# Performance work log

Hardware: AMD Instinct MI355X
Metric: run time of the kernel (lower is better)

## Reference

```python
import jax, jax.numpy as jnp
import numpy as np

N_RBF = 32
EPS_DIST = 0.01
R_RBF_MAX = 5.0
POWERS = (1.0, -1.0)


def _rbf_features(dist):
    # dist: [..., ] -> [..., N_RBF]; Gaussian-on-distance 'soft one-hot'
    q = jnp.linspace(0.0, 1.0, N_RBF).astype(dist.dtype)
    mu = q ** 2 * R_RBF_MAX
    sigma = (1.0 + R_RBF_MAX * q) / 7.0
    d = dist[..., None]
    return d ** 2 * jnp.exp(-d - ((d - mu) / sigma) ** 2)


def _pair_features(diff, dist):
    # RBF (32) + distance powers (2) + raw differences (3) = 37 features
    f_dist = jnp.stack(
        [dist ** n if n > 0 else 1.0 / (dist ** (-n) + EPS_DIST) for n in POWERS],
        axis=-1,
    )
    return jnp.concatenate([_rbf_features(dist), f_dist, diff], axis=-1)


def _mlp(x, Ws, bs):
    # MLP with linear_out=False: activation applied after every layer incl. last
    for W, b in zip(Ws, bs):
        x = jax.nn.silu(x @ W + b)
    return x


def setup_inputs() -> dict:
    key = jax.random.key(0)
    ks = jax.random.split(key, 6)
    B, N, M = 2048, 32, 8
    D_PAIR = N_RBF + 2 + 3  # 37
    H, F1, F_ION = 128, 128, 32
    r = jax.random.normal(ks[0], (B, N, 3), jnp.float32) * 2.0
    R = jax.random.normal(ks[1], (M, 3), jnp.float32) * 3.0
    Z = jnp.arange(1, M + 1, dtype=jnp.float32)
    init = lambda k, s: (jax.random.normal(k, s, jnp.float32) / np.sqrt(s[0])).astype(jnp.float32)
    return dict(
        r=r, R=R, Z=Z,
        W0=init(ks[2], (D_PAIR, H)), b0=jnp.zeros((H,), jnp.float32),
        W1=init(ks[3], (H, F1)), b1=jnp.zeros((F1,), jnp.float32),
        Wion=init(ks[4], (1, F_ION)), bion=jnp.zeros((F_ION,), jnp.float32),
    )


def reference(r, R, Z, W0, b0, W1, b1, Wion, bion):
    B, N = r.shape[0], r.shape[1]
    # --- pairwise diffs / distances ---
    diff_el_el = r[..., :, None, :] - r[..., None, :, :]          # [B,N,N,3]
    eye = jnp.eye(N, dtype=r.dtype)
    # safe sqrt on the diagonal (grad-safe), diagonal distance forced to 0
    dist_el_el = jnp.sqrt(jnp.sum(diff_el_el ** 2, axis=-1) + eye) * (1.0 - eye)  # [B,N,N]
    diff_el_ion = r[..., :, None, :] - R                           # [B,N,M,3]
    dist_el_ion = jnp.sqrt(jnp.sum(diff_el_ion ** 2, axis=-1))     # [B,N,M]

    # --- per-edge features ---
    features_el_el = _pair_features(diff_el_el, dist_el_el)        # [B,N,N,37]
    features_el_ion = _pair_features(diff_el_ion, dist_el_ion)     # [B,N,M,37]

    # --- edge MLP + sum aggregation over ions ---
    h = _mlp(features_el_ion, [W0, W1], [b0, b1])                  # [B,N,M,128]
    one_el = jnp.sum(h, axis=-2)                                   # [B,N,128]
    concat_ei = jnp.reshape(features_el_ion, features_el_ion.shape[:-2] + (-1,))  # [B,N,M*37]
    features_el = jnp.concatenate([one_el, concat_ei], axis=-1)    # [B,N,128+M*37]

    # --- ion features ---
    Zt = jnp.tile(Z, (B, 1))                                       # [B,M]
    features_ion = jax.nn.silu(Zt[..., None] @ Wion + bion)        # [B,M,32]
    return (features_el, features_ion)
```

## Files before the change

### kernel.cpp

```cpp
#include <hip/hip_runtime.h>


typedef __attribute__((ext_vector_type(8))) short short8;
typedef __attribute__((ext_vector_type(4))) float f32x4;

#define ITERS     8
#define UNITS_IT  16
#define ROWLEN    424
#define OUT_EL    27787264

__device__ __forceinline__ unsigned short f2bf(float f){
    unsigned int u = __builtin_bit_cast(unsigned int, f);
    u += 0x7fffu + ((u >> 16) & 1u);
    return (unsigned short)(u >> 16);
}
__device__ __forceinline__ unsigned int cvtpk_bf16(float lo, float hi){
    unsigned int r;
    asm("v_cvt_pk_bf16_f32 %0, %1, %2" : "=v"(r) : "v"(lo), "v"(hi));
    return r;
}
__device__ __forceinline__ unsigned short bf16s(float x){
    return (unsigned short)cvtpk_bf16(x, x);
}
__device__ __forceinline__ float fast_silu(float x){
    return x * __builtin_amdgcn_rcpf(1.0f + __expf(-x));
}

__global__ __launch_bounds__(512, 4)
void el_kernel(const float* __restrict__ r,
               const float* __restrict__ Rion,
               const float* __restrict__ W0,
               const float* __restrict__ b0,
               const float* __restrict__ W1,
               const float* __restrict__ b1,
               float* __restrict__ out)
{
    __shared__ __align__(16) unsigned short W0L[8][2][64][8];
    __shared__ __align__(16) unsigned short W1L[8][4][64][8];
    __shared__ __align__(16) unsigned short UNI[8][2048];

    const int t    = threadIdx.x;
    const int lane = t & 63;
    const int w    = t >> 6;
    const int quad = lane >> 4;
    const int l16  = lane & 15;

    for (int i = t; i < 8*2*64*8; i += 512){
        int j = i & 7, ln = (i >> 3) & 63, ch = (i >> 9) & 1, tc = i >> 10;
        int q = ln >> 4, n = tc*16 + (ln & 15);
        float v = 0.f;
        if (ch == 0)            v = W0[(q*8 + j)*128 + n];
        else if (q == 0){
            if      (j < 5)     v = W0[(32 + j)*128 + n];
            else if (j == 5)    v = b0[n];
        }
        ((unsigned short*)W0L)[i] = f2bf(v);
    }
    for (int i = t; i < 8*4*64*8; i += 512){
        int j = i & 7, ln = (i >> 3) & 63, c = (i >> 9) & 3, tc = i >> 11;
        int k = c*32 + (ln >> 4)*8 + j, n = tc*16 + (ln & 15);
        ((unsigned short*)W1L)[i] = f2bf(W1[k*128 + n]);
    }
    if (t < 128){
        UNI[t >> 4][512 + (t & 15)*8 + 5] = 0x3F80;
        UNI[t >> 4][512 + (t & 15)*8 + 6] = 0;
        UNI[t >> 4][512 + (t & 15)*8 + 7] = 0;
    }

    const int frow  = t >> 2;
    const int phase = t & 3;
    const int ul    = frow >> 3;
    const int m     = frow & 7;
    const int e16   = frow & 15;
    const float Rx = Rion[m*3+0];
    const float Ry = Rion[m*3+1];
    const float Rz = Rion[m*3+2];

    unsigned short* const uw = &UNI[w][0];
    const int h0row = l16 * 128;
    const int swz   = (l16 & 7) << 3;

    const f32x4 zeroc = {0.f,0.f,0.f,0.f};

    float bias1[8];
    #pragma unroll
    for (int tc = 0; tc < 8; ++tc) bias1[tc] = b1[tc*16 + l16];

    __syncthreads();

    const int ubase0 = blockIdx.x * (UNITS_IT * ITERS);

    for (int it = 0; it < ITERS; ++it){
        const int ubase = ubase0 + it * UNITS_IT;

        {
            int gu = ubase + ul;
            float dx = r[gu*3+0] - Rx;
            float dy = r[gu*3+1] - Ry;
            float dz = r[gu*3+2] - Rz;
            float d2 = dx*dx + dy*dy + dz*dz;
            float d  = __builtin_amdgcn_sqrtf(d2);
            float* orow = &out[(size_t)gu*ROWLEN + 128 + m*37];
            for (int f = phase; f < 37; f += 4){
                float val;
                if (f < 32){
                    float q  = (float)f * (1.0f/31.0f);
                    float mu = q*q*5.0f;
                    float is = 7.0f * __builtin_amdgcn_rcpf(1.0f + 5.0f*q);
                    float uu = (d - mu) * is;
                    val = d2 * __expf(-d - uu*uu);
                } else if (f == 32) val = d;
                else if (f == 33)   val = __builtin_amdgcn_rcpf(d + 0.01f);
                else if (f == 34)   val = dx;
                else if (f == 35)   val = dy;
                else                val = dz;
                orow[f] = val;
                unsigned short ub = bf16s(val);
                if (f < 32) uw[(f >> 3)*128 + e16*8 + (f & 7)] = ub;
                else        uw[512 + e16*8 + (f - 32)]          = ub;
            }
            if (phase == 3) uw[512 + e16*8 + 5] = 0x3F80;
        }

        short8 bf0 = *(const short8*)&uw[quad*128 + l16*8];
        short8 bf1 = *(const short8*)&uw[512 + l16*8];
        #pragma unroll
        for (int tc = 0; tc < 8; ++tc){
            short8 a0 = *(const short8*)&W0L[tc][0][lane][0];
            short8 a1 = *(const short8*)&W0L[tc][1][lane][0];
            f32x4 acc = __builtin_amdgcn_mfma_f32_16x16x32_bf16(a0, bf0, zeroc, 0, 0, 0);
            acc       = __builtin_amdgcn_mfma_f32_16x16x32_bf16(a1, bf1, acc,   0, 0, 0);
            unsigned int p01 = cvtpk_bf16(fast_silu(acc[0]), fast_silu(acc[1]));
            unsigned int p23 = cvtpk_bf16(fast_silu(acc[2]), fast_silu(acc[3]));
            unsigned long long pk = (unsigned long long)p01 |
                                    ((unsigned long long)p23 << 32);
            *(unsigned long long*)&uw[h0row + ((tc*16 + quad*4) ^ swz)] = pk;
        }

        short8 afk[4];
        #pragma unroll
        for (int c = 0; c < 4; ++c)
            afk[c] = *(const short8*)&uw[h0row + ((c*32 + quad*8) ^ swz)];

        f32x4 acc1[8];
        #pragma unroll
        for (int i = 0; i < 8; ++i) acc1[i] = zeroc;
        #pragma unroll
        for (int c = 0; c < 4; ++c){
            #pragma unroll
            for (int tc = 0; tc < 8; ++tc){
                short8 bw = *(const short8*)&W1L[tc][c][lane][0];
                acc1[tc] = __builtin_amdgcn_mfma_f32_16x16x32_bf16(afk[c], bw, acc1[tc], 0, 0, 0);
            }
        }
        #pragma unroll
        for (int tc = 0; tc < 8; ++tc){
            float v = 0.f;
            #pragma unroll
            for (int rr = 0; rr < 4; ++rr) v += fast_silu(acc1[tc][rr] + bias1[tc]);
            v += __shfl_xor(v, 16, 64);
            if ((quad & 1) == 0){
                size_t gu = (size_t)(ubase + 2*w + (quad >> 1));
                out[gu*ROWLEN + tc*16 + l16] = v;
            }
        }
    }
}

__global__ __launch_bounds__(256)
void ion_kernel(const float* __restrict__ Z,
                const float* __restrict__ Wion,
                const float* __restrict__ bion,
                float* __restrict__ out1)
{
    int gid = blockIdx.x*256 + threadIdx.x;
    int e0 = gid*4;
    float4 v;
    float* pv = &v.x;
    #pragma unroll
    for (int qi = 0; qi < 4; ++qi){
        int e = e0 + qi;
        int j = e & 31, mm = (e >> 5) & 7;
        pv[qi] = fast_silu(Z[mm] * Wion[j] + bion[j]);
    }
    *(float4*)&out1[e0] = v;
}

extern "C" void kernel_launch(void* const* d_in, const int* in_sizes, int n_in,
                              void* d_out, int out_size, void* d_ws, size_t ws_size,
                              hipStream_t stream)
{
    const float* r    = (const float*)d_in[0];
    const float* Rion = (const float*)d_in[1];
    const float* Z    = (const float*)d_in[2];
    const float* W0   = (const float*)d_in[3];
    const float* b0   = (const float*)d_in[4];
    const float* W1   = (const float*)d_in[5];
    const float* b1   = (const float*)d_in[6];
    const float* Wion = (const float*)d_in[7];
    const float* bion = (const float*)d_in[8];
    float* out = (float*)d_out;

    el_kernel<<<dim3(512), dim3(512), 0, stream>>>(r, Rion, W0, b0, W1, b1, out);
    ion_kernel<<<dim3(512), dim3(256), 0, stream>>>(Z, Wion, bion, out + OUT_EL);
}
```

Baseline: 188.9 us.

## Fuse ion kernel into edge kernel, prefetch positions, precompute RBF constants, raise MFMA priority

The ion-feature computation moves into the edge kernel, which drops a second launch. Each block's 512 threads write 2 elements apiece over 512 blocks, which covers all 2048*8*32 ion outputs. The next iteration's electron coordinates are prefetched into registers to hide global load latency. The per-feature RBF centres and inverse widths are precomputed once per thread, and the 37-feature loop becomes a fully unrolled 8-step loop plus a per-phase tail. s_setprio is raised around the second-layer MFMA loop, which could change wave scheduling fairness.

```diff
diff --git a/kernel.cpp b/kernel.cpp
--- a/kernel.cpp
+++ b/kernel.cpp
@@ -33,6 +33,9 @@
                const float* __restrict__ b0,
                const float* __restrict__ W1,
                const float* __restrict__ b1,
+               const float* __restrict__ Z,
+               const float* __restrict__ Wion,
+               const float* __restrict__ bion,
                float* __restrict__ out)
 {
     __shared__ __align__(16) unsigned short W0L[8][2][64][8];
@@ -67,6 +70,16 @@
         UNI[t >> 4][512 + (t & 15)*8 + 7] = 0;
     }
 
+    {
+        int e0 = (blockIdx.x*512 + t)*2;
+        int j0 = e0 & 31, mm = (e0 >> 5) & 7;
+        float z = Z[mm];
+        float2 v;
+        v.x = fast_silu(z * Wion[j0]     + bion[j0]);
+        v.y = fast_silu(z * Wion[j0 + 1] + bion[j0 + 1]);
+        *(float2*)&out[OUT_EL + e0] = v;
+    }
+
     const int frow  = t >> 2;
     const int phase = t & 3;
     const int ul    = frow >> 3;
@@ -86,40 +99,60 @@
     #pragma unroll
     for (int tc = 0; tc < 8; ++tc) bias1[tc] = b1[tc*16 + l16];
 
+    float muA[8], isA[8];
+    #pragma unroll
+    for (int k = 0; k < 8; ++k){
+        float q = (float)(phase + 4*k) * (1.0f/31.0f);
+        muA[k] = q*q*5.0f;
+        isA[k] = 7.0f * __builtin_amdgcn_rcpf(1.0f + 5.0f*q);
+    }
+
+    const int ubase0 = blockIdx.x * (UNITS_IT * ITERS);
+
+    float cx, cy, cz;
+    {
+        int gu = ubase0 + ul;
+        cx = r[gu*3+0]; cy = r[gu*3+1]; cz = r[gu*3+2];
+    }
+
     __syncthreads();
-
-    const int ubase0 = blockIdx.x * (UNITS_IT * ITERS);
 
     for (int it = 0; it < ITERS; ++it){
         const int ubase = ubase0 + it * UNITS_IT;
 
+        float nx = 0.f, ny = 0.f, nz = 0.f;
+        if (it < ITERS-1){
+            int gun = ubase + UNITS_IT + ul;
+            nx = r[gun*3+0]; ny = r[gun*3+1]; nz = r[gun*3+2];
+        }
+
         {
             int gu = ubase + ul;
-            float dx = r[gu*3+0] - Rx;
-            float dy = r[gu*3+1] - Ry;
-            float dz = r[gu*3+2] - Rz;
+            float dx = cx - Rx;
+            float dy = cy - Ry;
+            float dz = cz - Rz;
             float d2 = dx*dx + dy*dy + dz*dz;
             float d  = __builtin_amdgcn_sqrtf(d2);
             float* orow = &out[(size_t)gu*ROWLEN + 128 + m*37];
-            for (int f = phase; f < 37; f += 4){
-                float val;
-                if (f < 32){
-                    float q  = (float)f * (1.0f/31.0f);
-                    float mu = q*q*5.0f;
-                    float is = 7.0f * __builtin_amdgcn_rcpf(1.0f + 5.0f*q);
-                    float uu = (d - mu) * is;
-                    val = d2 * __expf(-d - uu*uu);
-                } else if (f == 32) val = d;
-                else if (f == 33)   val = __builtin_amdgcn_rcpf(d + 0.01f);
-                else if (f == 34)   val = dx;
-                else if (f == 35)   val = dy;
-                else                val = dz;
-                orow[f] = val;
-                unsigned short ub = bf16s(val);
-                if (f < 32) uw[(f >> 3)*128 + e16*8 + (f & 7)] = ub;
-                else        uw[512 + e16*8 + (f - 32)]          = ub;
-            }
-            if (phase == 3) uw[512 + e16*8 + 5] = 0x3F80;
+            #pragma unroll
+            for (int k = 0; k < 8; ++k){
+                float uu  = (d - muA[k]) * isA[k];
+                float val = d2 * __expf(-d - uu*uu);
+                orow[phase + 4*k] = val;
+                uw[(k >> 1)*128 + e16*8 + phase + ((k & 1) << 2)] = bf16s(val);
+            }
+            if (phase == 0){
+                orow[32] = d;  uw[512 + e16*8 + 0] = bf16s(d);
+                orow[36] = dz; uw[512 + e16*8 + 4] = bf16s(dz);
+            } else if (phase == 1){
+                float v = __builtin_amdgcn_rcpf(d + 0.01f);
+                orow[33] = v;  uw[512 + e16*8 + 1] = bf16s(v);
+            } else if (phase == 2){
+                orow[34] = dx; uw[512 + e16*8 + 2] = bf16s(dx);
+            } else {
+                orow[35] = dy; uw[512 + e16*8 + 3] = bf16s(dy);
+                uw[512 + e16*8 + 5] = 0x3F80;
+            }
         }
 
         short8 bf0 = *(const short8*)&uw[quad*128 + l16*8];
@@ -145,6 +178,7 @@
         f32x4 acc1[8];
         #pragma unroll
         for (int i = 0; i < 8; ++i) acc1[i] = zeroc;
+        __builtin_amdgcn_s_setprio(1);
         #pragma unroll
         for (int c = 0; c < 4; ++c){
             #pragma unroll
@@ -153,6 +187,7 @@
                 acc1[tc] = __builtin_amdgcn_mfma_f32_16x16x32_bf16(afk[c], bw, acc1[tc], 0, 0, 0);
             }
         }
+        __builtin_amdgcn_s_setprio(0);
         #pragma unroll
         for (int tc = 0; tc < 8; ++tc){
             float v = 0.f;
@@ -164,26 +199,9 @@
                 out[gu*ROWLEN + tc*16 + l16] = v;
             }
         }
-    }
-}
-
-__global__ __launch_bounds__(256)
-void ion_kernel(const float* __restrict__ Z,
-                const float* __restrict__ Wion,
-                const float* __restrict__ bion,
-                float* __restrict__ out1)
-{
-    int gid = blockIdx.x*256 + threadIdx.x;
-    int e0 = gid*4;
-    float4 v;
-    float* pv = &v.x;
-    #pragma unroll
-    for (int qi = 0; qi < 4; ++qi){
-        int e = e0 + qi;
-        int j = e & 31, mm = (e >> 5) & 7;
-        pv[qi] = fast_silu(Z[mm] * Wion[j] + bion[j]);
-    }
-    *(float4*)&out1[e0] = v;
+
+        cx = nx; cy = ny; cz = nz;
+    }
 }
 
 extern "C" void kernel_launch(void* const* d_in, const int* in_sizes, int n_in,
@@ -201,6 +219,6 @@
     const float* bion = (const float*)d_in[8];
     float* out = (float*)d_out;
 
-    el_kernel<<<dim3(512), dim3(512), 0, stream>>>(r, Rion, W0, b0, W1, b1, out);
-    ion_kernel<<<dim3(512), dim3(256), 0, stream>>>(Z, Wion, bion, out + OUT_EL);
-}
+    el_kernel<<<dim3(512), dim3(512), 0, stream>>>(r, Rion, W0, b0, W1, b1,
+                                                   Z, Wion, bion, out);
+}
```

After: 181.6 us. 1.04x faster.
